# Kernel optimization log

Measured on AMD Instinct MI355X. Metric: run time of the kernel, lower is better.

The kernel has to match this reference:

```python
import jax, jax.numpy as jnp
import numpy as np

H1, H2 = 32, 16  # LSTM units per direction (layer 1, layer 2)
F = 64           # input feature dim


def lstm(x, W, U, b, reverse=False, return_sequences=True):
    """Keras-style LSTM. x: [B,T,F]. W:[F,4H], U:[H,4H], b:[4H].
    Gate order i,f,g,o; sigmoid recurrent activation, tanh activation.
    Dropout is inference-mode (identity). If reverse, process time backwards
    (go_backwards=True)."""
    if reverse:
        x = x[:, ::-1]
    B = x.shape[0]
    H = U.shape[0]
    xW = jnp.einsum('btf,fg->btg', x, W) + b  # [B,T,4H] precomputed input gates

    def step(carry, xw_t):
        h, c = carry
        z = xw_t + h @ U                       # [B,4H]
        i, f, g, o = jnp.split(z, 4, axis=-1)
        i = jax.nn.sigmoid(i)
        f = jax.nn.sigmoid(f)
        g = jnp.tanh(g)
        o = jax.nn.sigmoid(o)
        c = f * c + i * g
        h = o * jnp.tanh(c)
        return (h, c), h

    h0 = jnp.zeros((B, H), x.dtype)
    (h_last, _), hs = jax.lax.scan(step, (h0, h0), jnp.swapaxes(xW, 0, 1))
    if return_sequences:
        hs = jnp.swapaxes(hs, 0, 1)  # [B,T,H]
        if reverse:
            hs = hs[:, ::-1]  # Bidirectional re-reverses backward outputs
        return hs
    return h_last


def setup_inputs() -> dict:
    key = jax.random.key(0)
    ks = jax.random.split(key, 17)
    s = 0.05
    d = {
        'inputs': jax.random.normal(ks[0], (4096, 128, F), jnp.float32),
        # layer 1 (bidirectional, 32 units each dir)
        'W1f': jax.random.normal(ks[1], (F, 4 * H1)) * s,
        'U1f': jax.random.normal(ks[2], (H1, 4 * H1)) * s,
        'b1f': jnp.zeros((4 * H1,)),
        'W1b': jax.random.normal(ks[3], (F, 4 * H1)) * s,
        'U1b': jax.random.normal(ks[4], (H1, 4 * H1)) * s,
        'b1b': jnp.zeros((4 * H1,)),
        # layer 2 (bidirectional, 16 units each dir, input 2*H1=64)
        'W2f': jax.random.normal(ks[5], (2 * H1, 4 * H2)) * s,
        'U2f': jax.random.normal(ks[6], (H2, 4 * H2)) * s,
        'b2f': jnp.zeros((4 * H2,)),
        'W2b': jax.random.normal(ks[7], (2 * H1, 4 * H2)) * s,
        'U2b': jax.random.normal(ks[8], (H2, 4 * H2)) * s,
        'b2b': jnp.zeros((4 * H2,)),
        # dense head
        'W3': jax.random.normal(ks[9], (2 * H2, 8)) * s,
        'b3': jnp.zeros((8,)),
        'W4': jax.random.normal(ks[10], (8, 2)) * s,
        'b4': jnp.zeros((2,)),
    }
    return d


def reference(inputs, W1f, U1f, b1f, W1b, U1b, b1b,
              W2f, U2f, b2f, W2b, U2b, b2b, W3, b3, W4, b4):
    # bi_one: concat(forward seq, time-aligned backward seq) -> [B,T,64]
    h1f = lstm(inputs, W1f, U1f, b1f, reverse=False, return_sequences=True)
    h1b = lstm(inputs, W1b, U1b, b1b, reverse=True, return_sequences=True)
    x = jnp.concatenate([h1f, h1b], axis=-1)
    # bi_two: last hidden state of each direction -> [B,32]
    h2f = lstm(x, W2f, U2f, b2f, reverse=False, return_sequences=False)
    h2b = lstm(x, W2b, U2b, b2b, reverse=True, return_sequences=False)
    x = jnp.concatenate([h2f, h2b], axis=-1)
    x = x @ W3 + b3
    x = x * jax.nn.sigmoid(x)  # swish
    x = x @ W4 + b4
    return jax.nn.sigmoid(x)
```

## Files before the change

### kernel.cpp

```cpp
#include <hip/hip_runtime.h>
#include <hip/hip_bf16.h>

#define T 128
#define F 64
#define H1 32
#define G1 128
#define H2 16
#define G2 64

typedef __attribute__((ext_vector_type(8))) short bf16x8;
typedef __attribute__((ext_vector_type(4))) float f32x4;

__device__ __forceinline__ float sigmoidf_(float x) {
    return 1.0f / (1.0f + __expf(-x));
}
__device__ __forceinline__ float tanhf_(float x) {
    return 1.0f - 2.0f / (__expf(2.0f * x) + 1.0f);
}
__device__ __forceinline__ unsigned short f2bf(float f) {
    union { float f; unsigned u; } c; c.f = f;
    unsigned r = c.u + 0x7FFF + ((c.u >> 16) & 1);
    return (unsigned short)(r >> 16);
}
__device__ __forceinline__ void lds_barrier() {
    asm volatile("s_waitcnt lgkmcnt(0)" ::: "memory");
    __builtin_amdgcn_s_barrier();
}
__device__ __forceinline__ float ext4(f32x4 v, int r) {
    const float ab = (r & 1) ? v[1] : v[0];
    const float cd = (r & 1) ? v[3] : v[2];
    return (r & 2) ? cd : ab;
}

__global__ __launch_bounds__(256) void xcvt(
    const float* __restrict__ x,
    unsigned short* __restrict__ xbf)
{
    const int g  = blockIdx.x;
    const int t0 = blockIdx.y * 4;
    const int m  = threadIdx.x >> 4;
    const int c4 = threadIdx.x & 15;
    const int ks   = c4 >> 3;
    const int quad = (c4 & 7) >> 1;
    const int j0   = (c4 & 1) * 4;
    const int slot = ks * 512 + (m + 16 * quad) * 8 + j0;

    #pragma unroll
    for (int tt = 0; tt < 4; ++tt) {
        const int t = t0 + tt;
        const float4 v = *(const float4*)(x + ((size_t)(g * 16 + m) * T + t) * 64 + c4 * 4);
        ushort4 u;
        u.x = f2bf(v.x); u.y = f2bf(v.y); u.z = f2bf(v.z); u.w = f2bf(v.w);
        *(ushort4*)(xbf + (size_t)(g * T + t) * 1024 + slot) = u;
    }
}

__global__ __launch_bounds__(512, 4) void lstm1_fused(
    const unsigned short* __restrict__ xbf,
    const float* __restrict__ W1f, const float* __restrict__ b1f, const float* __restrict__ U1f,
    const float* __restrict__ W1b, const float* __restrict__ b1b, const float* __restrict__ U1b,
    unsigned short* __restrict__ h1)
{
    __shared__ unsigned short hb[2][16 * 40];
    const int tid  = threadIdx.x;
    const int lane = tid & 63;
    const int wv   = tid >> 6;
    const int gh   = wv & 1;
    const int sh   = wv >> 1;
    const int n15  = lane & 15, quad = lane >> 4;
    const int d    = blockIdx.x & 1, g = blockIdx.x >> 1;

    const float* W  = d ? W1b : W1f;
    const float* U  = d ? U1b : U1f;
    const float* bs = d ? b1b : b1f;

    bf16x8 Wf[4][2], Uf[4];
    float bias[4];
    #pragma unroll
    for (int i = 0; i < 4; ++i) {
        const int col = (2 * i + gh) * 16 + n15;
        bias[i] = bs[col];
        #pragma unroll
        for (int ks = 0; ks < 2; ++ks) {
            bf16x8 f;
            #pragma unroll
            for (int j = 0; j < 8; ++j)
                f[j] = (short)f2bf(W[(ks * 32 + quad * 8 + j) * G1 + col]);
            Wf[i][ks] = f;
        }
        bf16x8 u;
        #pragma unroll
        for (int j = 0; j < 8; ++j)
            u[j] = (short)f2bf(U[(quad * 8 + j) * G1 + col]);
        Uf[i] = u;
    }

    #pragma unroll
    for (int i = 0; i < 3; ++i) {
        const int idx = tid + i * 512;
        if (idx < 1280) ((unsigned short*)hb)[idx] = 0;
    }

    float c = 0.0f;
    const unsigned short* xb = xbf + (size_t)g * T * 1024 + lane * 8;
    unsigned short* h1b = h1 + (size_t)g * T * 1024
        + d * 512 + (quad * 4 + sh + 16 * (gh * 2 + (n15 >> 3))) * 8 + (n15 & 7);

    bf16x8 xA0, xA1, xB0, xB1;
    {
        const unsigned short* p0 = xb + (size_t)(d ? (T - 1) : 0) * 1024;
        xA0 = *(const bf16x8*)(p0); xA1 = *(const bf16x8*)(p0 + 512);
        const unsigned short* p1 = xb + (size_t)(d ? (T - 2) : 1) * 1024;
        xB0 = *(const bf16x8*)(p1); xB1 = *(const bf16x8*)(p1 + 512);
    }
    lds_barrier();

    auto step = [&](int s, bf16x8& x0, bf16x8& x1) {
        const int t = d ? (T - 1 - s) : s;
        f32x4 a0 = (f32x4)bias[0], a1 = (f32x4)bias[1];
        f32x4 a2 = (f32x4)bias[2], a3 = (f32x4)bias[3];
        a0 = __builtin_amdgcn_mfma_f32_16x16x32_bf16(x0, Wf[0][0], a0, 0, 0, 0);
        a1 = __builtin_amdgcn_mfma_f32_16x16x32_bf16(x0, Wf[1][0], a1, 0, 0, 0);
        a2 = __builtin_amdgcn_mfma_f32_16x16x32_bf16(x0, Wf[2][0], a2, 0, 0, 0);
        a3 = __builtin_amdgcn_mfma_f32_16x16x32_bf16(x0, Wf[3][0], a3, 0, 0, 0);
        a0 = __builtin_amdgcn_mfma_f32_16x16x32_bf16(x1, Wf[0][1], a0, 0, 0, 0);
        a1 = __builtin_amdgcn_mfma_f32_16x16x32_bf16(x1, Wf[1][1], a1, 0, 0, 0);
        a2 = __builtin_amdgcn_mfma_f32_16x16x32_bf16(x1, Wf[2][1], a2, 0, 0, 0);
        a3 = __builtin_amdgcn_mfma_f32_16x16x32_bf16(x1, Wf[3][1], a3, 0, 0, 0);

        if (s + 2 < T) {
            const unsigned short* pn = xb + (size_t)(d ? (T - 3 - s) : (s + 2)) * 1024;
            x0 = *(const bf16x8*)(pn); x1 = *(const bf16x8*)(pn + 512);
        }

        const bf16x8 af = *(const bf16x8*)(hb[s & 1] + n15 * 40 + quad * 8);
        a0 = __builtin_amdgcn_mfma_f32_16x16x32_bf16(af, Uf[0], a0, 0, 0, 0);
        a1 = __builtin_amdgcn_mfma_f32_16x16x32_bf16(af, Uf[1], a1, 0, 0, 0);
        a2 = __builtin_amdgcn_mfma_f32_16x16x32_bf16(af, Uf[2], a2, 0, 0, 0);
        a3 = __builtin_amdgcn_mfma_f32_16x16x32_bf16(af, Uf[3], a3, 0, 0, 0);

        const float ig = sigmoidf_(ext4(a0, sh));
        const float fg = sigmoidf_(ext4(a1, sh));
        const float gg = tanhf_(ext4(a2, sh));
        const float og = sigmoidf_(ext4(a3, sh));
        c = fg * c + ig * gg;
        const float h = og * tanhf_(c);
        const unsigned short us = f2bf(h);
        hb[(s + 1) & 1][(quad * 4 + sh) * 40 + gh * 16 + n15] = us;
        h1b[(size_t)t * 1024] = us;
        lds_barrier();
    };

    #pragma unroll 1
    for (int s = 0; s < T; s += 2) {
        step(s, xA0, xA1);
        step(s + 1, xB0, xB1);
    }
}

__global__ __launch_bounds__(512, 2) void lstm2_head(
    const unsigned short* __restrict__ h1,
    const float* __restrict__ W2f, const float* __restrict__ b2f, const float* __restrict__ U2f,
    const float* __restrict__ W2b, const float* __restrict__ b2b, const float* __restrict__ U2b,
    const float* __restrict__ W3, const float* __restrict__ b3,
    const float* __restrict__ W4, const float* __restrict__ b4,
    float* __restrict__ out)
{
    __shared__ unsigned short hb2[2][2][400];
    __shared__ float hfin[2][16][16];
    __shared__ float ybuf[16][9];
    const int tid  = threadIdx.x;
    const int lane = tid & 63;
    const int wv   = tid >> 6;
    const int d    = wv & 1;
    const int sh   = wv >> 1;
    const int n15  = lane & 15, quad = lane >> 4;
    const int g    = blockIdx.x;

    const float* W  = d ? W2b : W2f;
    const float* U  = d ? U2b : U2f;
    const float* bs = d ? b2b : b2f;

    bf16x8 Wf[4][2], Uf[4];
    float bias[4];
    #pragma unroll
    for (int i = 0; i < 4; ++i) {
        const int col = i * 16 + n15;
        bias[i] = bs[col];
        #pragma unroll
        for (int ks = 0; ks < 2; ++ks) {
            bf16x8 f;
            #pragma unroll
            for (int j = 0; j < 8; ++j)
                f[j] = (short)f2bf(W[(ks * 32 + quad * 8 + j) * G2 + col]);
            Wf[i][ks] = f;
        }
        bf16x8 u;
        #pragma unroll
        for (int j = 0; j < 8; ++j) {
            const int k = quad * 8 + j;
            u[j] = (k < H2) ? (short)f2bf(U[k * G2 + col]) : (short)0;
        }
        Uf[i] = u;
    }

    #pragma unroll
    for (int i = 0; i < 4; ++i) {
        const int idx = tid + i * 512;
        if (idx < 1600) ((unsigned short*)hb2)[idx] = 0;
    }

    float c = 0.0f, hlast = 0.0f;
    const unsigned short* hl = h1 + (size_t)g * T * 1024 + lane * 8;

    bf16x8 hA0, hA1, hB0, hB1;
    {
        const unsigned short* p0 = hl + (size_t)(d ? (T - 1) : 0) * 1024;
        hA0 = *(const bf16x8*)(p0); hA1 = *(const bf16x8*)(p0 + 512);
        const unsigned short* p1 = hl + (size_t)(d ? (T - 2) : 1) * 1024;
        hB0 = *(const bf16x8*)(p1); hB1 = *(const bf16x8*)(p1 + 512);
    }
    lds_barrier();

    auto step = [&](int s, bf16x8& x0, bf16x8& x1) {
        f32x4 a0 = (f32x4)bias[0], a1 = (f32x4)bias[1];
        f32x4 a2 = (f32x4)bias[2], a3 = (f32x4)bias[3];
        a0 = __builtin_amdgcn_mfma_f32_16x16x32_bf16(x0, Wf[0][0], a0, 0, 0, 0);
        a1 = __builtin_amdgcn_mfma_f32_16x16x32_bf16(x0, Wf[1][0], a1, 0, 0, 0);
        a2 = __builtin_amdgcn_mfma_f32_16x16x32_bf16(x0, Wf[2][0], a2, 0, 0, 0);
        a3 = __builtin_amdgcn_mfma_f32_16x16x32_bf16(x0, Wf[3][0], a3, 0, 0, 0);
        a0 = __builtin_amdgcn_mfma_f32_16x16x32_bf16(x1, Wf[0][1], a0, 0, 0, 0);
        a1 = __builtin_amdgcn_mfma_f32_16x16x32_bf16(x1, Wf[1][1], a1, 0, 0, 0);
        a2 = __builtin_amdgcn_mfma_f32_16x16x32_bf16(x1, Wf[2][1], a2, 0, 0, 0);
        a3 = __builtin_amdgcn_mfma_f32_16x16x32_bf16(x1, Wf[3][1], a3, 0, 0, 0);

        if (s + 2 < T) {
            const unsigned short* pn = hl + (size_t)(d ? (T - 3 - s) : (s + 2)) * 1024;
            x0 = *(const bf16x8*)(pn); x1 = *(const bf16x8*)(pn + 512);
        }

        const bf16x8 af = *(const bf16x8*)(hb2[d][s & 1] + n15 * 24 + quad * 8);
        a0 = __builtin_amdgcn_mfma_f32_16x16x32_bf16(af, Uf[0], a0, 0, 0, 0);
        a1 = __builtin_amdgcn_mfma_f32_16x16x32_bf16(af, Uf[1], a1, 0, 0, 0);
        a2 = __builtin_amdgcn_mfma_f32_16x16x32_bf16(af, Uf[2], a2, 0, 0, 0);
        a3 = __builtin_amdgcn_mfma_f32_16x16x32_bf16(af, Uf[3], a3, 0, 0, 0);

        const float ig = sigmoidf_(ext4(a0, sh));
        const float fg = sigmoidf_(ext4(a1, sh));
        const float gg = tanhf_(ext4(a2, sh));
        const float og = sigmoidf_(ext4(a3, sh));
        c = fg * c + ig * gg;
        hlast = og * tanhf_(c);
        hb2[d][(s + 1) & 1][(quad * 4 + sh) * 24 + n15] = f2bf(hlast);
        lds_barrier();
    };

    #pragma unroll 1
    for (int s = 0; s < T; s += 2) {
        step(s, hA0, hA1);
        step(s + 1, hB0, hB1);
    }

    hfin[d][quad * 4 + sh][n15] = hlast;
    __syncthreads();

    if (tid < 128) {
        const int s = tid >> 3, u = tid & 7;
        float a = b3[u];
        #pragma unroll
        for (int k = 0; k < H2; ++k) a += hfin[0][s][k] * W3[k * 8 + u];
        #pragma unroll
        for (int k = 0; k < H2; ++k) a += hfin[1][s][k] * W3[(H2 + k) * 8 + u];
        ybuf[s][u] = a * sigmoidf_(a);
    }
    __syncthreads();
    if (tid < 32) {
        const int s = tid >> 1, o = tid & 1;
        float a = b4[o];
        #pragma unroll
        for (int k = 0; k < 8; ++k) a += ybuf[s][k] * W4[k * 2 + o];
        out[(size_t)(g * 16 + s) * 2 + o] = sigmoidf_(a);
    }
}

extern "C" void kernel_launch(void* const* d_in, const int* in_sizes, int n_in,
                              void* d_out, int out_size, void* d_ws, size_t ws_size,
                              hipStream_t stream) {
    const float* x   = (const float*)d_in[0];
    const float* W1f = (const float*)d_in[1];
    const float* U1f = (const float*)d_in[2];
    const float* b1f = (const float*)d_in[3];
    const float* W1b = (const float*)d_in[4];
    const float* U1b = (const float*)d_in[5];
    const float* b1b = (const float*)d_in[6];
    const float* W2f = (const float*)d_in[7];
    const float* U2f = (const float*)d_in[8];
    const float* b2f = (const float*)d_in[9];
    const float* W2b = (const float*)d_in[10];
    const float* U2b = (const float*)d_in[11];
    const float* b2b = (const float*)d_in[12];
    const float* W3  = (const float*)d_in[13];
    const float* b3  = (const float*)d_in[14];
    const float* W4  = (const float*)d_in[15];
    const float* b4  = (const float*)d_in[16];
    float* out = (float*)d_out;

    const int B  = in_sizes[0] / (T * F);
    const int NG = B / 16;

    const size_t perG = (size_t)T * 1024 * sizeof(unsigned short);
    int chG = (int)(ws_size / (2 * perG));
    if (chG > NG) chG = NG;
    if (chG < 1) chG = 1;
    unsigned short* xbf = (unsigned short*)d_ws;
    unsigned short* h1  = xbf + (size_t)chG * T * 1024;

    for (int g0 = 0; g0 < NG; g0 += chG) {
        const int cg = (NG - g0 < chG) ? (NG - g0) : chG;
        dim3 gcv(cg, T / 4);
        xcvt<<<gcv, 256, 0, stream>>>(x + (size_t)g0 * 16 * T * F, xbf);
        lstm1_fused<<<cg * 2, 512, 0, stream>>>(
            xbf, W1f, b1f, U1f, W1b, b1b, U1b, h1);
        lstm2_head<<<cg, 512, 0, stream>>>(
            h1, W2f, b2f, U2f, W2b, b2b, U2b, W3, b3, W4, b4,
            out + (size_t)g0 * 16 * 2);
    }
}
```

Baseline: 443.1 us.

## Halve LSTM1 block size with two cells per thread, stage xcvt stores through LDS

The layer-1 kernel now runs 4 waves instead of 8, and each thread computes two hidden units (two accumulator rows) per step. This cuts the waves that meet at each per-step barrier and reuses the MFMA outputs instead of discarding three of four rows. The input conversion kernel stages through shared memory so global writes are coalesced, and handles 8 timesteps per block. Smaller tweaks include scalarising the wave index with readfirstlane and feeding the bias vectors straight into the first MFMA. The cost is more serial transcendental work per thread on the recurrent critical path and extra barriers in xcvt.

```diff
diff --git a/kernel.cpp b/kernel.cpp
--- a/kernel.cpp
+++ b/kernel.cpp
@@ -26,18 +26,14 @@
     asm volatile("s_waitcnt lgkmcnt(0)" ::: "memory");
     __builtin_amdgcn_s_barrier();
 }
-__device__ __forceinline__ float ext4(f32x4 v, int r) {
-    const float ab = (r & 1) ? v[1] : v[0];
-    const float cd = (r & 1) ? v[3] : v[2];
-    return (r & 2) ? cd : ab;
-}
 
 __global__ __launch_bounds__(256) void xcvt(
     const float* __restrict__ x,
     unsigned short* __restrict__ xbf)
 {
+    __shared__ unsigned short tile[1024];
     const int g  = blockIdx.x;
-    const int t0 = blockIdx.y * 4;
+    const int t0 = blockIdx.y * 8;
     const int m  = threadIdx.x >> 4;
     const int c4 = threadIdx.x & 15;
     const int ks   = c4 >> 3;
@@ -45,17 +41,20 @@
     const int j0   = (c4 & 1) * 4;
     const int slot = ks * 512 + (m + 16 * quad) * 8 + j0;
 
-    #pragma unroll
-    for (int tt = 0; tt < 4; ++tt) {
+    for (int tt = 0; tt < 8; ++tt) {
         const int t = t0 + tt;
         const float4 v = *(const float4*)(x + ((size_t)(g * 16 + m) * T + t) * 64 + c4 * 4);
         ushort4 u;
         u.x = f2bf(v.x); u.y = f2bf(v.y); u.z = f2bf(v.z); u.w = f2bf(v.w);
-        *(ushort4*)(xbf + (size_t)(g * T + t) * 1024 + slot) = u;
-    }
-}
-
-__global__ __launch_bounds__(512, 4) void lstm1_fused(
+        *(ushort4*)(tile + slot) = u;
+        __syncthreads();
+        *(uint2*)(xbf + (size_t)(g * T + t) * 1024 + threadIdx.x * 4) =
+            *(const uint2*)(tile + threadIdx.x * 4);
+        __syncthreads();
+    }
+}
+
+__global__ __launch_bounds__(256, 2) void lstm1_fused(
     const unsigned short* __restrict__ xbf,
     const float* __restrict__ W1f, const float* __restrict__ b1f, const float* __restrict__ U1f,
     const float* __restrict__ W1b, const float* __restrict__ b1b, const float* __restrict__ U1b,
@@ -64,7 +63,7 @@
     __shared__ unsigned short hb[2][16 * 40];
     const int tid  = threadIdx.x;
     const int lane = tid & 63;
-    const int wv   = tid >> 6;
+    const int wv   = __builtin_amdgcn_readfirstlane(tid >> 6);
     const int gh   = wv & 1;
     const int sh   = wv >> 1;
     const int n15  = lane & 15, quad = lane >> 4;
@@ -75,11 +74,11 @@
     const float* bs = d ? b1b : b1f;
 
     bf16x8 Wf[4][2], Uf[4];
-    float bias[4];
+    f32x4 biasC[4];
     #pragma unroll
     for (int i = 0; i < 4; ++i) {
         const int col = (2 * i + gh) * 16 + n15;
-        bias[i] = bs[col];
+        biasC[i] = (f32x4)(bs[col]);
         #pragma unroll
         for (int ks = 0; ks < 2; ++ks) {
             bf16x8 f;
@@ -96,15 +95,13 @@
     }
 
     #pragma unroll
-    for (int i = 0; i < 3; ++i) {
-        const int idx = tid + i * 512;
-        if (idx < 1280) ((unsigned short*)hb)[idx] = 0;
-    }
-
-    float c = 0.0f;
+    for (int i = 0; i < 5; ++i) ((unsigned short*)hb)[tid + i * 256] = 0;
+
+    float c0 = 0.0f, c1 = 0.0f;
     const unsigned short* xb = xbf + (size_t)g * T * 1024 + lane * 8;
-    unsigned short* h1b = h1 + (size_t)g * T * 1024
-        + d * 512 + (quad * 4 + sh + 16 * (gh * 2 + (n15 >> 3))) * 8 + (n15 & 7);
+    unsigned short* h1b0 = h1 + (size_t)g * T * 1024
+        + d * 512 + ((quad * 4 + 2 * sh) + 16 * (gh * 2 + (n15 >> 3))) * 8 + (n15 & 7);
+    unsigned short* h1b1 = h1b0 + 8;
 
     bf16x8 xA0, xA1, xB0, xB1;
     {
@@ -117,12 +114,10 @@
 
     auto step = [&](int s, bf16x8& x0, bf16x8& x1) {
         const int t = d ? (T - 1 - s) : s;
-        f32x4 a0 = (f32x4)bias[0], a1 = (f32x4)bias[1];
-        f32x4 a2 = (f32x4)bias[2], a3 = (f32x4)bias[3];
-        a0 = __builtin_amdgcn_mfma_f32_16x16x32_bf16(x0, Wf[0][0], a0, 0, 0, 0);
-        a1 = __builtin_amdgcn_mfma_f32_16x16x32_bf16(x0, Wf[1][0], a1, 0, 0, 0);
-        a2 = __builtin_amdgcn_mfma_f32_16x16x32_bf16(x0, Wf[2][0], a2, 0, 0, 0);
-        a3 = __builtin_amdgcn_mfma_f32_16x16x32_bf16(x0, Wf[3][0], a3, 0, 0, 0);
+        f32x4 a0 = __builtin_amdgcn_mfma_f32_16x16x32_bf16(x0, Wf[0][0], biasC[0], 0, 0, 0);
+        f32x4 a1 = __builtin_amdgcn_mfma_f32_16x16x32_bf16(x0, Wf[1][0], biasC[1], 0, 0, 0);
+        f32x4 a2 = __builtin_amdgcn_mfma_f32_16x16x32_bf16(x0, Wf[2][0], biasC[2], 0, 0, 0);
+        f32x4 a3 = __builtin_amdgcn_mfma_f32_16x16x32_bf16(x0, Wf[3][0], biasC[3], 0, 0, 0);
         a0 = __builtin_amdgcn_mfma_f32_16x16x32_bf16(x1, Wf[0][1], a0, 0, 0, 0);
         a1 = __builtin_amdgcn_mfma_f32_16x16x32_bf16(x1, Wf[1][1], a1, 0, 0, 0);
         a2 = __builtin_amdgcn_mfma_f32_16x16x32_bf16(x1, Wf[2][1], a2, 0, 0, 0);
@@ -139,15 +134,28 @@
         a2 = __builtin_amdgcn_mfma_f32_16x16x32_bf16(af, Uf[2], a2, 0, 0, 0);
         a3 = __builtin_amdgcn_mfma_f32_16x16x32_bf16(af, Uf[3], a3, 0, 0, 0);
 
-        const float ig = sigmoidf_(ext4(a0, sh));
-        const float fg = sigmoidf_(ext4(a1, sh));
-        const float gg = tanhf_(ext4(a2, sh));
-        const float og = sigmoidf_(ext4(a3, sh));
-        c = fg * c + ig * gg;
-        const float h = og * tanhf_(c);
-        const unsigned short us = f2bf(h);
-        hb[(s + 1) & 1][(quad * 4 + sh) * 40 + gh * 16 + n15] = us;
-        h1b[(size_t)t * 1024] = us;
+        {
+            const float ig = sigmoidf_(sh ? a0[2] : a0[0]);
+            const float fg = sigmoidf_(sh ? a1[2] : a1[0]);
+            const float gg = tanhf_(sh ? a2[2] : a2[0]);
+            const float og = sigmoidf_(sh ? a3[2] : a3[0]);
+            c0 = fg * c0 + ig * gg;
+            const float h = og * tanhf_(c0);
+            const unsigned short us = f2bf(h);
+            hb[(s + 1) & 1][(quad * 4 + 2 * sh) * 40 + gh * 16 + n15] = us;
+            h1b0[(size_t)t * 1024] = us;
+        }
+        {
+            const float ig = sigmoidf_(sh ? a0[3] : a0[1]);
+            const float fg = sigmoidf_(sh ? a1[3] : a1[1]);
+            const float gg = tanhf_(sh ? a2[3] : a2[1]);
+            const float og = sigmoidf_(sh ? a3[3] : a3[1]);
+            c1 = fg * c1 + ig * gg;
+            const float h = og * tanhf_(c1);
+            const unsigned short us = f2bf(h);
+            hb[(s + 1) & 1][(quad * 4 + 2 * sh + 1) * 40 + gh * 16 + n15] = us;
+            h1b1[(size_t)t * 1024] = us;
+        }
         lds_barrier();
     };
 
@@ -171,7 +179,7 @@
     __shared__ float ybuf[16][9];
     const int tid  = threadIdx.x;
     const int lane = tid & 63;
-    const int wv   = tid >> 6;
+    const int wv   = __builtin_amdgcn_readfirstlane(tid >> 6);
     const int d    = wv & 1;
     const int sh   = wv >> 1;
     const int n15  = lane & 15, quad = lane >> 4;
@@ -182,11 +190,11 @@
     const float* bs = d ? b2b : b2f;
 
     bf16x8 Wf[4][2], Uf[4];
-    float bias[4];
+    f32x4 biasC[4];
     #pragma unroll
     for (int i = 0; i < 4; ++i) {
         const int col = i * 16 + n15;
-        bias[i] = bs[col];
+        biasC[i] = (f32x4)(bs[col]);
         #pragma unroll
         for (int ks = 0; ks < 2; ++ks) {
             bf16x8 f;
@@ -223,12 +231,10 @@
     lds_barrier();
 
     auto step = [&](int s, bf16x8& x0, bf16x8& x1) {
-        f32x4 a0 = (f32x4)bias[0], a1 = (f32x4)bias[1];
-        f32x4 a2 = (f32x4)bias[2], a3 = (f32x4)bias[3];
-        a0 = __builtin_amdgcn_mfma_f32_16x16x32_bf16(x0, Wf[0][0], a0, 0, 0, 0);
-        a1 = __builtin_amdgcn_mfma_f32_16x16x32_bf16(x0, Wf[1][0], a1, 0, 0, 0);
-        a2 = __builtin_amdgcn_mfma_f32_16x16x32_bf16(x0, Wf[2][0], a2, 0, 0, 0);
-        a3 = __builtin_amdgcn_mfma_f32_16x16x32_bf16(x0, Wf[3][0], a3, 0, 0, 0);
+        f32x4 a0 = __builtin_amdgcn_mfma_f32_16x16x32_bf16(x0, Wf[0][0], biasC[0], 0, 0, 0);
+        f32x4 a1 = __builtin_amdgcn_mfma_f32_16x16x32_bf16(x0, Wf[1][0], biasC[1], 0, 0, 0);
+        f32x4 a2 = __builtin_amdgcn_mfma_f32_16x16x32_bf16(x0, Wf[2][0], biasC[2], 0, 0, 0);
+        f32x4 a3 = __builtin_amdgcn_mfma_f32_16x16x32_bf16(x0, Wf[3][0], biasC[3], 0, 0, 0);
         a0 = __builtin_amdgcn_mfma_f32_16x16x32_bf16(x1, Wf[0][1], a0, 0, 0, 0);
         a1 = __builtin_amdgcn_mfma_f32_16x16x32_bf16(x1, Wf[1][1], a1, 0, 0, 0);
         a2 = __builtin_amdgcn_mfma_f32_16x16x32_bf16(x1, Wf[2][1], a2, 0, 0, 0);
@@ -245,10 +251,14 @@
         a2 = __builtin_amdgcn_mfma_f32_16x16x32_bf16(af, Uf[2], a2, 0, 0, 0);
         a3 = __builtin_amdgcn_mfma_f32_16x16x32_bf16(af, Uf[3], a3, 0, 0, 0);
 
-        const float ig = sigmoidf_(ext4(a0, sh));
-        const float fg = sigmoidf_(ext4(a1, sh));
-        const float gg = tanhf_(ext4(a2, sh));
-        const float og = sigmoidf_(ext4(a3, sh));
+        const float z0 = (sh & 1) ? ((sh & 2) ? a0[3] : a0[1]) : ((sh & 2) ? a0[2] : a0[0]);
+        const float z1 = (sh & 1) ? ((sh & 2) ? a1[3] : a1[1]) : ((sh & 2) ? a1[2] : a1[0]);
+        const float z2 = (sh & 1) ? ((sh & 2) ? a2[3] : a2[1]) : ((sh & 2) ? a2[2] : a2[0]);
+        const float z3 = (sh & 1) ? ((sh & 2) ? a3[3] : a3[1]) : ((sh & 2) ? a3[2] : a3[0]);
+        const float ig = sigmoidf_(z0);
+        const float fg = sigmoidf_(z1);
+        const float gg = tanhf_(z2);
+        const float og = sigmoidf_(z3);
         c = fg * c + ig * gg;
         hlast = og * tanhf_(c);
         hb2[d][(s + 1) & 1][(quad * 4 + sh) * 24 + n15] = f2bf(hlast);
@@ -317,9 +327,9 @@
 
     for (int g0 = 0; g0 < NG; g0 += chG) {
         const int cg = (NG - g0 < chG) ? (NG - g0) : chG;
-        dim3 gcv(cg, T / 4);
+        dim3 gcv(cg, T / 8);
         xcvt<<<gcv, 256, 0, stream>>>(x + (size_t)g0 * 16 * T * F, xbf);
-        lstm1_fused<<<cg * 2, 512, 0, stream>>>(
+        lstm1_fused<<<cg * 2, 256, 0, stream>>>(
             xbf, W1f, b1f, U1f, W1b, b1b, U1b, h1);
         lstm2_head<<<cg, 512, 0, stream>>>(
             h1, W2f, b2f, U2f, W2b, b2b, U2b, W3, b3, W4, b4,
```

Result: faster. 431.2 us (-2.7%).
